# Kernel tuning notes

Hardware: AMD Instinct MI355X
Metric: run time of the kernel (lower is better)

The kernel has to match this reference:

```python
import jax, jax.numpy as jnp
import numpy as np

D_MODEL = 1024
N_HEADS = 16
D_K = D_MODEL // N_HEADS
D_FF = 4096
EPS = 1e-5


def _layernorm(x, g, b):
    mu = jnp.mean(x, axis=-1, keepdims=True)
    var = jnp.mean(jnp.square(x - mu), axis=-1, keepdims=True)
    return (x - mu) * jax.lax.rsqrt(var + EPS) * g + b


def setup_inputs() -> dict:
    key = jax.random.key(0)
    ks = jax.random.split(key, 16)
    s = 0.02
    B, S = 2, 2048
    inp = {
        "x": jax.random.normal(ks[0], (B, S, D_MODEL), dtype=jnp.float32),
        "mask": jnp.ones((1, 1, S, S), dtype=jnp.int32),
        # attention projections (stored [in, out]; y = x @ W + b)
        "Wq": jax.random.normal(ks[1], (D_MODEL, D_MODEL)) * s,
        "bq": jnp.zeros((D_MODEL,)),
        "Wk": jax.random.normal(ks[2], (D_MODEL, D_MODEL)) * s,
        "bk": jnp.zeros((D_MODEL,)),
        "Wv": jax.random.normal(ks[3], (D_MODEL, D_MODEL)) * s,
        "bv": jnp.zeros((D_MODEL,)),
        "Wo": jax.random.normal(ks[4], (D_MODEL, D_MODEL)) * s,
        "bo": jnp.zeros((D_MODEL,)),
        "temperature": jnp.sqrt(jnp.array([float(D_K)], dtype=jnp.float32)),
        "time_weights": jax.random.normal(ks[5], (1, N_HEADS, 1, D_K)),
        "gateW": jax.random.normal(ks[6], (D_K, 1)) * s,
        "gateb": jnp.zeros((1,)),
        "ln_attn_g": jnp.ones((D_MODEL,)),
        "ln_attn_b": jnp.zeros((D_MODEL,)),
        # feed-forward
        "fc1W": jax.random.normal(ks[7], (D_MODEL, D_FF)) * s,
        "fc1b": jnp.zeros((D_FF,)),
        "fc2W": jax.random.normal(ks[8], (D_FF, D_MODEL)) * s,
        "fc2b": jnp.zeros((D_MODEL,)),
        "n1g": jnp.ones((D_MODEL,)),
        "n1b": jnp.zeros((D_MODEL,)),
        "n2g": jnp.ones((D_MODEL,)),
        "n2b": jnp.zeros((D_MODEL,)),
    }
    return inp


def reference(x, mask, Wq, bq, Wk, bk, Wv, bv, Wo, bo, temperature,
              time_weights, gateW, gateb, ln_attn_g, ln_attn_b,
              fc1W, fc1b, fc2W, fc2b, n1g, n1b, n2g, n2b):
    B, S, D = x.shape
    H, dk = N_HEADS, D_K

    def heads(t):  # [B,S,D] -> [B,H,S,dk]
        return t.reshape(B, S, H, dk).transpose(0, 2, 1, 3)

    q = heads(x @ Wq + bq) + time_weights  # learned per-head bias on Q
    k = heads(x @ Wk + bk)
    v = heads(x @ Wv + bv)

    scores = jnp.einsum("bhqd,bhkd->bhqk", q, k) / temperature
    scores = jnp.where(mask == 0, jnp.float32(-1e9), scores)
    gate = jax.nn.sigmoid(q @ gateW + gateb)  # [B,H,S,1] per-query gate
    scores = scores * gate
    probs = jax.nn.softmax(scores, axis=-1)

    ctx = jnp.einsum("bhqk,bhkd->bhqd", probs, v)
    ctx = ctx.transpose(0, 2, 1, 3).reshape(B, S, D)
    attn_out = _layernorm(ctx @ Wo + bo, ln_attn_g, ln_attn_b)

    x1 = _layernorm(x + attn_out, n1g, n1b)
    ff = jax.nn.gelu(x1 @ fc1W + fc1b, approximate=False) @ fc2W + fc2b
    return _layernorm(x1 + ff, n2g, n2b)
```

## Files before the change

kernel.cpp:

```cpp
#include <hip/hip_runtime.h>
#include <stdint.h>
#include <math.h>


typedef uint16_t u16;
typedef unsigned long long u64;
typedef __attribute__((ext_vector_type(8))) short short8;
typedef __attribute__((ext_vector_type(4))) float f32x4;

#define S_LEN 2048
#define DM 1024

#define GLOAD_LDS16(g, l)                                                      \
  __builtin_amdgcn_global_load_lds(                                            \
      (const __attribute__((address_space(1))) void*)(g),                      \
      (__attribute__((address_space(3))) void*)(l), 16, 0, 0)

#define VM0_BARRIER()                                                          \
  do {                                                                         \
    asm volatile("s_waitcnt vmcnt(0)" ::: "memory");                           \
    __builtin_amdgcn_s_barrier();                                              \
  } while (0)

__device__ __forceinline__ float bf2f(u16 h) {
  union { uint32_t u; float f; } x;
  x.u = ((uint32_t)h) << 16;
  return x.f;
}
__device__ __forceinline__ u16 f2bf(float f) {
  union { float f; uint32_t u; } x;
  x.f = f;
  uint32_t r = (x.u + 0x7fffu + ((x.u >> 16) & 1u)) >> 16;
  return (u16)r;
}
__device__ __forceinline__ u16 f2bf_fast(float f) {
  union { float f; uint32_t u; } x;
  x.f = f;
  return (u16)((x.u + 0x8000u) >> 16);
}

__device__ __forceinline__ float gelu_ex(float v) {
  float x = fabsf(v) * 0.70710678118654752f;
  float t = __builtin_amdgcn_rcpf(__builtin_fmaf(0.3275911f, x, 1.0f));
  float p = 1.061405429f;
  p = __builtin_fmaf(p, t, -1.453152027f);
  p = __builtin_fmaf(p, t, 1.421413741f);
  p = __builtin_fmaf(p, t, -0.284496736f);
  p = __builtin_fmaf(p, t, 0.254829592f);
  p = p * t;
  float ex = __builtin_amdgcn_exp2f(-1.4426950408889634f * x * x);
  float er = __builtin_fmaf(-p, ex, 1.0f);
  er = (v < 0.f) ? -er : er;
  return 0.5f * v * (1.0f + er);
}

union U8 { uint4 u; u16 s[8]; };
union U4 { uint2 u; u16 s[4]; };

__global__ __launch_bounds__(256) void cvt_k(const float* __restrict__ in,
                                             u16* __restrict__ out, int n) {
  int i = (blockIdx.x * 256 + threadIdx.x) * 4;
  if (i >= n) return;
  float4 v = *(const float4*)(in + i);
  U4 o;
  o.s[0] = f2bf(v.x); o.s[1] = f2bf(v.y); o.s[2] = f2bf(v.z); o.s[3] = f2bf(v.w);
  *(uint2*)(out + i) = o.u;
}

__global__ __launch_bounds__(256) void mb_k(const int* __restrict__ mask,
                                            u16* __restrict__ mb) {
  int tid = blockIdx.x * 256 + threadIdx.x;
  const int* src = mask + (size_t)tid * 16;
  uint32_t b = 0;
#pragma unroll
  for (int q = 0; q < 4; q++) {
    int4 m = *(const int4*)(src + q * 4);
    b |= (m.x != 0 ? 1u : 0u) << (q * 4 + 0);
    b |= (m.y != 0 ? 1u : 0u) << (q * 4 + 1);
    b |= (m.z != 0 ? 1u : 0u) << (q * 4 + 2);
    b |= (m.w != 0 ? 1u : 0u) << (q * 4 + 3);
  }
  mb[tid] = (u16)b;
}

__device__ __forceinline__ void tcvt_body(const float* __restrict__ in,
                                          u16* __restrict__ out, int R, int C) {
  __shared__ u16 tile[64][72];
  int c0 = blockIdx.x * 64, r0 = blockIdx.y * 64;
  int t = threadIdx.x;
  int r = t & 63, seg = t >> 6;
  const float* src = in + (size_t)(r0 + r) * C + c0 + seg * 16;
#pragma unroll
  for (int q = 0; q < 4; q++) {
    float4 v = *(const float4*)(src + q * 4);
    tile[r][seg * 16 + q * 4 + 0] = f2bf(v.x);
    tile[r][seg * 16 + q * 4 + 1] = f2bf(v.y);
    tile[r][seg * 16 + q * 4 + 2] = f2bf(v.z);
    tile[r][seg * 16 + q * 4 + 3] = f2bf(v.w);
  }
  __syncthreads();
  U8 v0, v1;
#pragma unroll
  for (int i = 0; i < 8; i++) v0.s[i] = tile[seg * 16 + i][r];
#pragma unroll
  for (int i = 0; i < 8; i++) v1.s[i] = tile[seg * 16 + 8 + i][r];
  u16* dst = out + (size_t)(c0 + r) * R + r0 + seg * 16;
  *(uint4*)dst = v0.u;
  *(uint4*)(dst + 8) = v1.u;
}

__global__ __launch_bounds__(256) void transpose_cvt_k(const float* __restrict__ in,
                                                       u16* __restrict__ out,
                                                       int R, int C) {
  tcvt_body(in, out, R, C);
}

__global__ __launch_bounds__(256) void transpose_cvt3_k(const float* __restrict__ i0,
                                                        const float* __restrict__ i1,
                                                        const float* __restrict__ i2,
                                                        u16* __restrict__ o0,
                                                        u16* __restrict__ o1,
                                                        u16* __restrict__ o2) {
  int z = blockIdx.z;
  const float* in = (z == 0) ? i0 : (z == 1) ? i1 : i2;
  u16* out = (z == 0) ? o0 : (z == 1) ? o1 : o2;
  tcvt_body(in, out, 1024, 1024);
}

__global__ __launch_bounds__(256) void vtrans_k(const u16* __restrict__ V,
                                                u16* __restrict__ VT) {
  __shared__ u16 tile[64][72];
  int bx = blockIdx.x, bh = blockIdx.y;
  int b = bh >> 4, h = bh & 15;
  int t = threadIdx.x, r = t & 63, seg = t >> 6;
  const u16* src = V + (size_t)(b * S_LEN + bx * 64 + r) * DM + h * 64 + seg * 16;
  *(uint4*)&tile[r][seg * 16] = *(const uint4*)src;
  *(uint4*)&tile[r][seg * 16 + 8] = *(const uint4*)(src + 8);
  __syncthreads();
  U8 v0, v1;
#pragma unroll
  for (int i = 0; i < 8; i++) v0.s[i] = tile[seg * 16 + i][r];
#pragma unroll
  for (int i = 0; i < 8; i++) v1.s[i] = tile[seg * 16 + 8 + i][r];
  u16* dst = VT + ((size_t)bh * 64 + r) * S_LEN + bx * 64 + seg * 16;
  *(uint4*)dst = v0.u;
  *(uint4*)(dst + 8) = v1.u;
}

template <int BM, int EPI, int MXS>
__global__ __launch_bounds__(256) void gemm_bt(const u16* __restrict__ A,
                                               const u16* __restrict__ Bt,
                                               u16* __restrict__ C,
                                               const float* __restrict__ bias,
                                               int M, int N, int K) {
  constexpr int MI = BM / 32;
  constexpr int RPW = BM / 4;
  __shared__ u16 As[2][BM * 32];
  __shared__ u16 Bs[2][128 * 32];
  int t = threadIdx.x;
  int wid = t >> 6, lane = t & 63;
  int g = lane >> 4, li = lane & 15;
  int bx = MXS ? blockIdx.y : blockIdx.x;
  int by = MXS ? blockIdx.x : blockIdx.y;
  int wr = (wid >> 1) * (BM / 2), wc = (wid & 1) * 64;

  const u16* a0 = A + (size_t)(by * BM + wid * RPW + (lane >> 2)) * K + (lane & 3) * 8;
  const u16* b0 = Bt + (size_t)(bx * 128 + wid * 32 + (lane >> 2)) * K + (lane & 3) * 8;
  u16* lA[2] = {&As[0][wid * RPW * 32], &As[1][wid * RPW * 32]};
  u16* lB[2] = {&Bs[0][wid * 1024], &Bs[1][wid * 1024]};

  f32x4 acc[MI][4];
#pragma unroll
  for (int i = 0; i < MI; i++)
#pragma unroll
    for (int j = 0; j < 4; j++) acc[i][j] = (f32x4){0.f, 0.f, 0.f, 0.f};

  auto stage = [&](int buf, int kk) {
    GLOAD_LDS16(a0 + kk, lA[buf]);
    if (BM == 128) GLOAD_LDS16(a0 + (size_t)16 * K + kk, lA[buf] + 512);
    GLOAD_LDS16(b0 + kk, lB[buf]);
    GLOAD_LDS16(b0 + (size_t)16 * K + kk, lB[buf] + 512);
  };
  auto compute = [&](int buf) {
    short8 af[MI], bfv[4];
#pragma unroll
    for (int i = 0; i < MI; i++)
      af[i] = *(const short8*)&As[buf][(wr + i * 16 + li) * 32 + g * 8];
#pragma unroll
    for (int i = 0; i < 4; i++)
      bfv[i] = *(const short8*)&Bs[buf][(wc + i * 16 + li) * 32 + g * 8];
    __builtin_amdgcn_s_setprio(1);
#pragma unroll
    for (int mi = 0; mi < MI; mi++)
#pragma unroll
      for (int ni = 0; ni < 4; ni++)
        acc[mi][ni] = __builtin_amdgcn_mfma_f32_16x16x32_bf16(
            af[mi], bfv[ni], acc[mi][ni], 0, 0, 0);
    __builtin_amdgcn_s_setprio(0);
  };

  stage(0, 0);
  VM0_BARRIER();
  for (int k0 = 0; k0 < K; k0 += 64) {
    stage(1, k0 + 32);
    compute(0);
    VM0_BARRIER();
    if (k0 + 64 < K) stage(0, k0 + 64);
    compute(1);
    VM0_BARRIER();
  }

#pragma unroll
  for (int ni = 0; ni < 4; ni++) {
    int col = bx * 128 + wc + ni * 16 + li;
    float bv = bias[col];
#pragma unroll
    for (int mi = 0; mi < MI; mi++) {
#pragma unroll
      for (int r = 0; r < 4; r++) {
        int row = by * BM + wr + mi * 16 + g * 4 + r;
        float v = acc[mi][ni][r] + bv;
        if (EPI == 2) v = gelu_ex(v);
        C[(size_t)row * N + col] = f2bf(v);
      }
    }
  }
}

__global__ __launch_bounds__(256) void qkv_gemm(const u16* __restrict__ A,
                                                const u16* __restrict__ WTq,
                                                const u16* __restrict__ WTk,
                                                const u16* __restrict__ WTv,
                                                u16* __restrict__ Cq,
                                                u16* __restrict__ Ck,
                                                u16* __restrict__ Cv,
                                                const float* __restrict__ bq,
                                                const float* __restrict__ bk,
                                                const float* __restrict__ bv,
                                                const float* __restrict__ tw) {
  const int K = 1024, N = 1024;
  __shared__ u16 As[2][128 * 32];
  __shared__ u16 Bs[2][128 * 32];
  int t = threadIdx.x;
  int wid = t >> 6, lane = t & 63;
  int g = lane >> 4, li = lane & 15;
  int by = blockIdx.x, bx = blockIdx.y, z = blockIdx.z;
  int wr = (wid >> 1) * 64, wc = (wid & 1) * 64;

  const u16* Bt = (z == 0) ? WTq : (z == 1) ? WTk : WTv;
  u16* C = (z == 0) ? Cq : (z == 1) ? Ck : Cv;
  const float* bias = (z == 0) ? bq : (z == 1) ? bk : bv;

  const u16* a0 = A + (size_t)(by * 128 + wid * 32 + (lane >> 2)) * K + (lane & 3) * 8;
  const u16* b0 = Bt + (size_t)(bx * 128 + wid * 32 + (lane >> 2)) * K + (lane & 3) * 8;
  u16* lA[2] = {&As[0][wid * 1024], &As[1][wid * 1024]};
  u16* lB[2] = {&Bs[0][wid * 1024], &Bs[1][wid * 1024]};

  f32x4 acc[4][4];
#pragma unroll
  for (int i = 0; i < 4; i++)
#pragma unroll
    for (int j = 0; j < 4; j++) acc[i][j] = (f32x4){0.f, 0.f, 0.f, 0.f};

  auto stage = [&](int buf, int kk) {
    GLOAD_LDS16(a0 + kk, lA[buf]);
    GLOAD_LDS16(a0 + (size_t)16 * K + kk, lA[buf] + 512);
    GLOAD_LDS16(b0 + kk, lB[buf]);
    GLOAD_LDS16(b0 + (size_t)16 * K + kk, lB[buf] + 512);
  };
  auto compute = [&](int buf) {
    short8 af[4], bfv[4];
#pragma unroll
    for (int i = 0; i < 4; i++)
      af[i] = *(const short8*)&As[buf][(wr + i * 16 + li) * 32 + g * 8];
#pragma unroll
    for (int i = 0; i < 4; i++)
      bfv[i] = *(const short8*)&Bs[buf][(wc + i * 16 + li) * 32 + g * 8];
    __builtin_amdgcn_s_setprio(1);
#pragma unroll
    for (int mi = 0; mi < 4; mi++)
#pragma unroll
      for (int ni = 0; ni < 4; ni++)
        acc[mi][ni] = __builtin_amdgcn_mfma_f32_16x16x32_bf16(
            af[mi], bfv[ni], acc[mi][ni], 0, 0, 0);
    __builtin_amdgcn_s_setprio(0);
  };

  stage(0, 0);
  VM0_BARRIER();
  for (int k0 = 0; k0 < K; k0 += 64) {
    stage(1, k0 + 32);
    compute(0);
    VM0_BARRIER();
    if (k0 + 64 < K) stage(0, k0 + 64);
    compute(1);
    VM0_BARRIER();
  }

#pragma unroll
  for (int ni = 0; ni < 4; ni++) {
    int col = bx * 128 + wc + ni * 16 + li;
    float bvv = bias[col];
    if (z == 0) bvv += tw[col];
#pragma unroll
    for (int mi = 0; mi < 4; mi++) {
#pragma unroll
      for (int r = 0; r < 4; r++) {
        int row = by * 128 + wr + mi * 16 + g * 4 + r;
        C[(size_t)row * N + col] = f2bf(acc[mi][ni][r] + bvv);
      }
    }
  }
}

__global__ __launch_bounds__(256) void attn_k(const u16* __restrict__ Q,
                                              const u16* __restrict__ Kp,
                                              const u16* __restrict__ VT,
                                              u16* __restrict__ CTX,
                                              const u16* __restrict__ mb,
                                              const float* __restrict__ gateW,
                                              const float* __restrict__ gateb,
                                              const float* __restrict__ temp) {
  __shared__ u16 Qs[64][72];
  __shared__ u16 Ks[64][72];
  __shared__ u16 Vs[64][72];
  __shared__ u16 Ps[4][16][72];
  __shared__ float gate_s[64];

  int blk = blockIdx.x;
  int bh = blk & 31, qt = blk >> 5;
  int b = bh >> 4, h = bh & 15;
  int t = threadIdx.x, wid = t >> 6, lane = t & 63;
  int g = lane >> 4, li = lane & 15;
  int sq0 = qt * 64;

  const u16* Qb  = Q + ((size_t)b * S_LEN) * DM + h * 64;
  const u16* Kb  = Kp + ((size_t)b * S_LEN) * DM + h * 64;
  const u16* VTb = VT + ((size_t)(b * 16 + h) * 64) * S_LEN;

  {
    int r = t >> 2, cs = (t & 3) * 16;
    const u16* src = Qb + (size_t)(sq0 + r) * DM + cs;
    *(uint4*)&Qs[r][cs] = *(const uint4*)src;
    *(uint4*)&Qs[r][cs + 8] = *(const uint4*)(src + 8);
  }
  __syncthreads();
  if (t < 64) {
    float acc = gateb[0];
#pragma unroll
    for (int d = 0; d < 64; d++) acc += bf2f(Qs[t][d]) * gateW[d];
    gate_s[t] = 1.f / (1.f + __expf(-acc));
  }
  __syncthreads();

  const float LOG2E = 1.4426950408889634f;
  float invt2 = LOG2E / temp[0];
  const float NEG2 = -1.0e9f * 1.4426950408889634f;
  short8 qf0 = *(const short8*)&Qs[wid * 16 + li][g * 8];
  short8 qf1 = *(const short8*)&Qs[wid * 16 + li][32 + g * 8];
  float gqs[4], ng[4];
  int sq[4];
#pragma unroll
  for (int r = 0; r < 4; r++) {
    float gq = gate_s[wid * 16 + g * 4 + r];
    gqs[r] = gq * invt2;
    ng[r] = NEG2 * gq;
    sq[r] = sq0 + wid * 16 + g * 4 + r;
  }

  float m_i[4], psl[4];
  f32x4 o[4];
#pragma unroll
  for (int r = 0; r < 4; r++) { m_i[r] = -1e30f; psl[r] = 0.f; }
#pragma unroll
  for (int n = 0; n < 4; n++) o[n] = (f32x4){0.f, 0.f, 0.f, 0.f};

  for (int kt = 0; kt < 32; kt++) {
    __syncthreads();
    {
      int r = t >> 2, cs = (t & 3) * 16;
      const u16* srcK = Kb + (size_t)(kt * 64 + r) * DM + cs;
      *(uint4*)&Ks[r][cs] = *(const uint4*)srcK;
      *(uint4*)&Ks[r][cs + 8] = *(const uint4*)(srcK + 8);
      const u16* srcV = VTb + (size_t)r * S_LEN + kt * 64 + cs;
      *(uint4*)&Vs[r][cs] = *(const uint4*)srcV;
      *(uint4*)&Vs[r][cs + 8] = *(const uint4*)(srcV + 8);
    }
    u64 bits[4];
#pragma unroll
    for (int r = 0; r < 4; r++)
      bits[r] = *(const u64*)(mb + (size_t)sq[r] * 128 + kt * 4);
    __syncthreads();

    f32x4 sc[4];
#pragma unroll
    for (int ni = 0; ni < 4; ni++) {
      sc[ni] = (f32x4){0.f, 0.f, 0.f, 0.f};
      short8 kf0 = *(const short8*)&Ks[ni * 16 + li][g * 8];
      short8 kf1 = *(const short8*)&Ks[ni * 16 + li][32 + g * 8];
      sc[ni] = __builtin_amdgcn_mfma_f32_16x16x32_bf16(qf0, kf0, sc[ni], 0, 0, 0);
      sc[ni] = __builtin_amdgcn_mfma_f32_16x16x32_bf16(qf1, kf1, sc[ni], 0, 0, 0);
    }

    float sval[4][4];
    float rmax[4] = {-1e30f, -1e30f, -1e30f, -1e30f};
    bool allm = ((bits[0] & bits[1] & bits[2] & bits[3]) == ~0ull);
    if (__all(allm)) {
#pragma unroll
      for (int ni = 0; ni < 4; ni++)
#pragma unroll
        for (int r = 0; r < 4; r++) {
          float s = sc[ni][r] * gqs[r];
          sval[ni][r] = s;
          rmax[r] = fmaxf(rmax[r], s);
        }
    } else {
      u64 bs[4];
#pragma unroll
      for (int r = 0; r < 4; r++) bs[r] = bits[r] >> li;
#pragma unroll
      for (int ni = 0; ni < 4; ni++)
#pragma unroll
        for (int r = 0; r < 4; r++) {
          float s = ((bs[r] >> (ni * 16)) & 1ull) ? sc[ni][r] * gqs[r] : ng[r];
          sval[ni][r] = s;
          rmax[r] = fmaxf(rmax[r], s);
        }
    }
#pragma unroll
    for (int off = 1; off < 16; off <<= 1)
#pragma unroll
      for (int r = 0; r < 4; r++)
        rmax[r] = fmaxf(rmax[r], __shfl_xor(rmax[r], off, 64));

    float alpha[4];
#pragma unroll
    for (int r = 0; r < 4; r++) {
      float mnew = fmaxf(m_i[r], rmax[r]);
      alpha[r] = __builtin_amdgcn_exp2f(m_i[r] - mnew);
      m_i[r] = mnew;
    }
    float pp[4] = {0.f, 0.f, 0.f, 0.f};
#pragma unroll
    for (int ni = 0; ni < 4; ni++)
#pragma unroll
      for (int r = 0; r < 4; r++) {
        float p = __builtin_amdgcn_exp2f(sval[ni][r] - m_i[r]);
        pp[r] += p;
        Ps[wid][g * 4 + r][ni * 16 + li] = f2bf_fast(p);
      }
#pragma unroll
    for (int r = 0; r < 4; r++) psl[r] = psl[r] * alpha[r] + pp[r];
#pragma unroll
    for (int n = 0; n < 4; n++)
#pragma unroll
      for (int r = 0; r < 4; r++) o[n][r] *= alpha[r];

    __builtin_amdgcn_wave_barrier();

    short8 pf0 = *(const short8*)&Ps[wid][li][g * 8];
    short8 pf1 = *(const short8*)&Ps[wid][li][32 + g * 8];
#pragma unroll
    for (int ni = 0; ni < 4; ni++) {
      short8 vf0 = *(const short8*)&Vs[ni * 16 + li][g * 8];
      short8 vf1 = *(const short8*)&Vs[ni * 16 + li][32 + g * 8];
      o[ni] = __builtin_amdgcn_mfma_f32_16x16x32_bf16(pf0, vf0, o[ni], 0, 0, 0);
      o[ni] = __builtin_amdgcn_mfma_f32_16x16x32_bf16(pf1, vf1, o[ni], 0, 0, 0);
    }
  }

  float linv[4];
#pragma unroll
  for (int r = 0; r < 4; r++) {
    float l = psl[r];
#pragma unroll
    for (int off = 1; off < 16; off <<= 1) l += __shfl_xor(l, off, 64);
    linv[r] = 1.f / l;
  }
#pragma unroll
  for (int ni = 0; ni < 4; ni++) {
    int col = h * 64 + ni * 16 + li;
#pragma unroll
    for (int r = 0; r < 4; r++) {
      size_t row = (size_t)b * S_LEN + sq[r];
      CTX[row * DM + col] = f2bf(o[ni][r] * linv[r]);
    }
  }
}

__device__ __forceinline__ void block_sum2(float& a, float& b, float* red, int t) {
#pragma unroll
  for (int off = 32; off > 0; off >>= 1) {
    a += __shfl_xor(a, off, 64);
    b += __shfl_xor(b, off, 64);
  }
  __syncthreads();
  if ((t & 63) == 0) {
    red[(t >> 6) * 2] = a;
    red[(t >> 6) * 2 + 1] = b;
  }
  __syncthreads();
  a = red[0] + red[2] + red[4] + red[6];
  b = red[1] + red[3] + red[5] + red[7];
}

__global__ __launch_bounds__(256) void ln1_k(const u16* __restrict__ po,
                                             const float* __restrict__ x,
                                             const float* __restrict__ g1,
                                             const float* __restrict__ b1,
                                             const float* __restrict__ g2,
                                             const float* __restrict__ b2,
                                             u16* __restrict__ x1) {
  __shared__ float red[8];
  int row = blockIdx.x, t = threadIdx.x;
  size_t base = (size_t)row * 1024 + t * 4;
  U4 pv; pv.u = *(const uint2*)(po + base);
  float v[4];
#pragma unroll
  for (int i = 0; i < 4; i++) v[i] = bf2f(pv.s[i]);
  float s1 = v[0] + v[1] + v[2] + v[3];
  float s2 = v[0]*v[0] + v[1]*v[1] + v[2]*v[2] + v[3]*v[3];
  block_sum2(s1, s2, red, t);
  float mu = s1 * (1.f / 1024.f);
  float rs = rsqrtf(s2 * (1.f / 1024.f) - mu * mu + 1e-5f);
  float4 xv = *(const float4*)(x + base);
  float4 g1v = *(const float4*)(g1 + t * 4);
  float4 b1v = *(const float4*)(b1 + t * 4);
  float w[4];
  w[0] = xv.x + ((v[0] - mu) * rs * g1v.x + b1v.x);
  w[1] = xv.y + ((v[1] - mu) * rs * g1v.y + b1v.y);
  w[2] = xv.z + ((v[2] - mu) * rs * g1v.z + b1v.z);
  w[3] = xv.w + ((v[3] - mu) * rs * g1v.w + b1v.w);
  s1 = w[0] + w[1] + w[2] + w[3];
  s2 = w[0]*w[0] + w[1]*w[1] + w[2]*w[2] + w[3]*w[3];
  block_sum2(s1, s2, red, t);
  mu = s1 * (1.f / 1024.f);
  rs = rsqrtf(s2 * (1.f / 1024.f) - mu * mu + 1e-5f);
  float4 g2v = *(const float4*)(g2 + t * 4);
  float4 b2v = *(const float4*)(b2 + t * 4);
  U4 ov;
  ov.s[0] = f2bf((w[0] - mu) * rs * g2v.x + b2v.x);
  ov.s[1] = f2bf((w[1] - mu) * rs * g2v.y + b2v.y);
  ov.s[2] = f2bf((w[2] - mu) * rs * g2v.z + b2v.z);
  ov.s[3] = f2bf((w[3] - mu) * rs * g2v.w + b2v.w);
  *(uint2*)(x1 + base) = ov.u;
}

__global__ __launch_bounds__(256) void ln2_k(const u16* __restrict__ y,
                                             const u16* __restrict__ x1,
                                             const float* __restrict__ g,
                                             const float* __restrict__ b,
                                             float* __restrict__ out) {
  __shared__ float red[8];
  int row = blockIdx.x, t = threadIdx.x;
  size_t base = (size_t)row * 1024 + t * 4;
  U4 yv; yv.u = *(const uint2*)(y + base);
  U4 xv; xv.u = *(const uint2*)(x1 + base);
  float w[4];
#pragma unroll
  for (int i = 0; i < 4; i++) w[i] = bf2f(yv.s[i]) + bf2f(xv.s[i]);
  float s1 = w[0] + w[1] + w[2] + w[3];
  float s2 = w[0]*w[0] + w[1]*w[1] + w[2]*w[2] + w[3]*w[3];
  block_sum2(s1, s2, red, t);
  float mu = s1 * (1.f / 1024.f);
  float rs = rsqrtf(s2 * (1.f / 1024.f) - mu * mu + 1e-5f);
  float4 gv = *(const float4*)(g + t * 4);
  float4 bv = *(const float4*)(b + t * 4);
  float4 ov;
  ov.x = (w[0] - mu) * rs * gv.x + bv.x;
  ov.y = (w[1] - mu) * rs * gv.y + bv.y;
  ov.z = (w[2] - mu) * rs * gv.z + bv.z;
  ov.w = (w[3] - mu) * rs * gv.w + bv.w;
  *(float4*)(out + base) = ov;
}

extern "C" void kernel_launch(void* const* d_in, const int* in_sizes, int n_in,
                              void* d_out, int out_size, void* d_ws, size_t ws_size,
                              hipStream_t stream) {
  (void)in_sizes; (void)n_in; (void)out_size;
  const float* x    = (const float*)d_in[0];
  const int*   mask = (const int*)d_in[1];
  const float* Wq = (const float*)d_in[2];  const float* bq = (const float*)d_in[3];
  const float* Wk = (const float*)d_in[4];  const float* bk = (const float*)d_in[5];
  const float* Wv = (const float*)d_in[6];  const float* bv = (const float*)d_in[7];
  const float* Wo = (const float*)d_in[8];  const float* bo = (const float*)d_in[9];
  const float* temp = (const float*)d_in[10];
  const float* tw   = (const float*)d_in[11];
  const float* gW   = (const float*)d_in[12]; const float* gb  = (const float*)d_in[13];
  const float* lag  = (const float*)d_in[14]; const float* lab = (const float*)d_in[15];
  const float* f1W  = (const float*)d_in[16]; const float* f1b = (const float*)d_in[17];
  const float* f2W  = (const float*)d_in[18]; const float* f2b = (const float*)d_in[19];
  const float* n1g  = (const float*)d_in[20]; const float* n1b = (const float*)d_in[21];
  const float* n2g  = (const float*)d_in[22]; const float* n2b = (const float*)d_in[23];
  float* out = (float*)d_out;

  u16* ws = (u16*)d_ws;
  const size_t MB4 = (size_t)4096 * 1024;
  u16* s0 = ws;
  u16* s1 = ws + 1 * MB4;
  u16* s2 = ws + 2 * MB4;
  u16* s3 = ws + 3 * MB4;
  u16* s4 = ws + 4 * MB4;
  u16* d0 = (u16*)d_out;
  u16* d1 = d0 + MB4;
  bool bigws = ws_size >= (size_t)9 * 8 * 1024 * 1024;
  u16* Hfull = ws + 5 * MB4;

  dim3 blk(256);
  cvt_k<<<dim3(4096), blk, 0, stream>>>(x, s4, 4096 * 1024);
  transpose_cvt3_k<<<dim3(16, 16, 3), blk, 0, stream>>>(Wq, Wk, Wv, s0, s1, s2);
  qkv_gemm<<<dim3(32, 8, 3), blk, 0, stream>>>(s4, s0, s1, s2, s3, d0, d1,
                                               bq, bk, bv, tw);
  vtrans_k<<<dim3(32, 32), blk, 0, stream>>>(d1, s0);
  mb_k<<<dim3(1024), blk, 0, stream>>>(mask, s1);
  transpose_cvt_k<<<dim3(16, 16), blk, 0, stream>>>(Wo, s4, 1024, 1024);
  attn_k<<<dim3(1024), blk, 0, stream>>>(s3, d0, s0, s2, s1, gW, gb, temp);
  gemm_bt<64, 0, 1><<<dim3(64, 8), blk, 0, stream>>>(s2, s4, d0, bo, 4096, 1024, 1024);
  ln1_k<<<dim3(4096), blk, 0, stream>>>(d0, x, lag, lab, n1g, n1b, s3);
  transpose_cvt_k<<<dim3(64, 16), blk, 0, stream>>>(f1W, s0, 1024, 4096);
  transpose_cvt_k<<<dim3(16, 64), blk, 0, stream>>>(f2W, s1, 4096, 1024);
  if (bigws) {
    gemm_bt<128, 2, 0><<<dim3(32, 32), blk, 0, stream>>>(s3, s0, Hfull, f1b,
                                                         4096, 4096, 1024);
    gemm_bt<64, 0, 0><<<dim3(8, 64), blk, 0, stream>>>(Hfull, s1, s2, f2b,
                                                       4096, 1024, 4096);
  } else {
    for (int i = 0; i < 2; i++) {
      const u16* Ai = s3 + (size_t)i * 2048 * 1024;
      u16* Yi = s2 + (size_t)i * 2048 * 1024;
      gemm_bt<128, 2, 0><<<dim3(32, 16), blk, 0, stream>>>(Ai, s0, d0, f1b,
                                                           2048, 4096, 1024);
      gemm_bt<64, 0, 1><<<dim3(32, 8), blk, 0, stream>>>(d0, s1, Yi, f2b,
                                                         2048, 1024, 4096);
    }
  }
  ln2_k<<<dim3(4096), blk, 0, stream>>>(s2, s3, n2g, n2b, out);
}
```

Measured before the change: 461.3 us.

## Register-prefetch K/V tiles, share Q/P LDS buffer, lazy softmax rescale in attention

The attention kernel now loads the next K/V tile into registers while the current tile is computed, so global-load latency overlaps with MFMA work. The Q tile buffer is reused for the P tile once Q fragments are in registers, which cuts LDS use and allows a launch bound of 5 blocks per CU. The online-softmax rescale is skipped unless some row max rises by more than 8 in log2 units, and the gate dot product is spread over all threads with shuffles. The extra prefetch registers and the threshold-based rescale change register pressure and the numeric path.

```diff
diff --git a/kernel.cpp b/kernel.cpp
--- a/kernel.cpp
+++ b/kernel.cpp
@@ -313,18 +313,17 @@
   }
 }
 
-__global__ __launch_bounds__(256) void attn_k(const u16* __restrict__ Q,
-                                              const u16* __restrict__ Kp,
-                                              const u16* __restrict__ VT,
-                                              u16* __restrict__ CTX,
-                                              const u16* __restrict__ mb,
-                                              const float* __restrict__ gateW,
-                                              const float* __restrict__ gateb,
-                                              const float* __restrict__ temp) {
-  __shared__ u16 Qs[64][72];
+__global__ __launch_bounds__(256, 5) void attn_k(const u16* __restrict__ Q,
+                                                 const u16* __restrict__ Kp,
+                                                 const u16* __restrict__ VT,
+                                                 u16* __restrict__ CTX,
+                                                 const u16* __restrict__ mb,
+                                                 const float* __restrict__ gateW,
+                                                 const float* __restrict__ gateb,
+                                                 const float* __restrict__ temp) {
+  __shared__ u16 QPs[64 * 72];
   __shared__ u16 Ks[64][72];
   __shared__ u16 Vs[64][72];
-  __shared__ u16 Ps[4][16][72];
   __shared__ float gate_s[64];
 
   int blk = blockIdx.x;
@@ -333,40 +332,51 @@
   int t = threadIdx.x, wid = t >> 6, lane = t & 63;
   int g = lane >> 4, li = lane & 15;
   int sq0 = qt * 64;
+  int rr = t >> 2, cc = (t & 3) * 16;
 
   const u16* Qb  = Q + ((size_t)b * S_LEN) * DM + h * 64;
   const u16* Kb  = Kp + ((size_t)b * S_LEN) * DM + h * 64;
   const u16* VTb = VT + ((size_t)(b * 16 + h) * 64) * S_LEN;
 
   {
-    int r = t >> 2, cs = (t & 3) * 16;
-    const u16* src = Qb + (size_t)(sq0 + r) * DM + cs;
-    *(uint4*)&Qs[r][cs] = *(const uint4*)src;
-    *(uint4*)&Qs[r][cs + 8] = *(const uint4*)(src + 8);
+    const u16* src = Qb + (size_t)(sq0 + rr) * DM + cc;
+    *(uint4*)&QPs[rr * 72 + cc] = *(const uint4*)src;
+    *(uint4*)&QPs[rr * 72 + cc + 8] = *(const uint4*)(src + 8);
   }
   __syncthreads();
-  if (t < 64) {
-    float acc = gateb[0];
-#pragma unroll
-    for (int d = 0; d < 64; d++) acc += bf2f(Qs[t][d]) * gateW[d];
-    gate_s[t] = 1.f / (1.f + __expf(-acc));
+  {
+    U8 q0, q1;
+    q0.u = *(const uint4*)&QPs[rr * 72 + cc];
+    q1.u = *(const uint4*)&QPs[rr * 72 + cc + 8];
+    float4 w0 = *(const float4*)(gateW + cc);
+    float4 w1 = *(const float4*)(gateW + cc + 4);
+    float4 w2 = *(const float4*)(gateW + cc + 8);
+    float4 w3 = *(const float4*)(gateW + cc + 12);
+    float acc;
+    acc  = bf2f(q0.s[0]) * w0.x + bf2f(q0.s[1]) * w0.y +
+           bf2f(q0.s[2]) * w0.z + bf2f(q0.s[3]) * w0.w;
+    acc += bf2f(q0.s[4]) * w1.x + bf2f(q0.s[5]) * w1.y +
+           bf2f(q0.s[6]) * w1.z + bf2f(q0.s[7]) * w1.w;
+    acc += bf2f(q1.s[0]) * w2.x + bf2f(q1.s[1]) * w2.y +
+           bf2f(q1.s[2]) * w2.z + bf2f(q1.s[3]) * w2.w;
+    acc += bf2f(q1.s[4]) * w3.x + bf2f(q1.s[5]) * w3.y +
+           bf2f(q1.s[6]) * w3.z + bf2f(q1.s[7]) * w3.w;
+    acc += __shfl_xor(acc, 1, 64);
+    acc += __shfl_xor(acc, 2, 64);
+    if ((t & 3) == 0) gate_s[rr] = 1.f / (1.f + __expf(-(acc + gateb[0])));
   }
   __syncthreads();
 
   const float LOG2E = 1.4426950408889634f;
   float invt2 = LOG2E / temp[0];
-  const float NEG2 = -1.0e9f * 1.4426950408889634f;
-  short8 qf0 = *(const short8*)&Qs[wid * 16 + li][g * 8];
-  short8 qf1 = *(const short8*)&Qs[wid * 16 + li][32 + g * 8];
-  float gqs[4], ng[4];
-  int sq[4];
-#pragma unroll
-  for (int r = 0; r < 4; r++) {
-    float gq = gate_s[wid * 16 + g * 4 + r];
-    gqs[r] = gq * invt2;
-    ng[r] = NEG2 * gq;
-    sq[r] = sq0 + wid * 16 + g * 4 + r;
-  }
+  float cng = -1.0e9f * temp[0];
+  short8 qf0 = *(const short8*)&QPs[(wid * 16 + li) * 72 + g * 8];
+  short8 qf1 = *(const short8*)&QPs[(wid * 16 + li) * 72 + 32 + g * 8];
+  float gqs[4];
+  int row0 = sq0 + wid * 16 + g * 4;
+#pragma unroll
+  for (int r = 0; r < 4; r++) gqs[r] = gate_s[wid * 16 + g * 4 + r] * invt2;
+  const u16* mbp = mb + (size_t)row0 * 128;
 
   float m_i[4], psl[4];
   f32x4 o[4];
@@ -375,21 +385,30 @@
 #pragma unroll
   for (int n = 0; n < 4; n++) o[n] = (f32x4){0.f, 0.f, 0.f, 0.f};
 
+  uint4 kxa, kxb, vxa, vxb;
+  {
+    const u16* sK = Kb + (size_t)rr * DM + cc;
+    kxa = *(const uint4*)sK; kxb = *(const uint4*)(sK + 8);
+    const u16* sV = VTb + (size_t)rr * S_LEN + cc;
+    vxa = *(const uint4*)sV; vxb = *(const uint4*)(sV + 8);
+  }
+
   for (int kt = 0; kt < 32; kt++) {
     __syncthreads();
-    {
-      int r = t >> 2, cs = (t & 3) * 16;
-      const u16* srcK = Kb + (size_t)(kt * 64 + r) * DM + cs;
-      *(uint4*)&Ks[r][cs] = *(const uint4*)srcK;
-      *(uint4*)&Ks[r][cs + 8] = *(const uint4*)(srcK + 8);
-      const u16* srcV = VTb + (size_t)r * S_LEN + kt * 64 + cs;
-      *(uint4*)&Vs[r][cs] = *(const uint4*)srcV;
-      *(uint4*)&Vs[r][cs + 8] = *(const uint4*)(srcV + 8);
-    }
+    *(uint4*)&Ks[rr][cc]     = kxa;
+    *(uint4*)&Ks[rr][cc + 8] = kxb;
+    *(uint4*)&Vs[rr][cc]     = vxa;
+    *(uint4*)&Vs[rr][cc + 8] = vxb;
     u64 bits[4];
 #pragma unroll
     for (int r = 0; r < 4; r++)
-      bits[r] = *(const u64*)(mb + (size_t)sq[r] * 128 + kt * 4);
+      bits[r] = *(const u64*)(mbp + (size_t)r * 128 + kt * 4);
+    if (kt + 1 < 32) {
+      const u16* sK = Kb + (size_t)((kt + 1) * 64 + rr) * DM + cc;
+      kxa = *(const uint4*)sK; kxb = *(const uint4*)(sK + 8);
+      const u16* sV = VTb + (size_t)rr * S_LEN + (kt + 1) * 64 + cc;
+      vxa = *(const uint4*)sV; vxb = *(const uint4*)(sV + 8);
+    }
     __syncthreads();
 
     f32x4 sc[4];
@@ -402,7 +421,6 @@
       sc[ni] = __builtin_amdgcn_mfma_f32_16x16x32_bf16(qf1, kf1, sc[ni], 0, 0, 0);
     }
 
-    float sval[4][4];
     float rmax[4] = {-1e30f, -1e30f, -1e30f, -1e30f};
     bool allm = ((bits[0] & bits[1] & bits[2] & bits[3]) == ~0ull);
     if (__all(allm)) {
@@ -411,7 +429,7 @@
 #pragma unroll
         for (int r = 0; r < 4; r++) {
           float s = sc[ni][r] * gqs[r];
-          sval[ni][r] = s;
+          sc[ni][r] = s;
           rmax[r] = fmaxf(rmax[r], s);
         }
     } else {
@@ -422,8 +440,9 @@
       for (int ni = 0; ni < 4; ni++)
 #pragma unroll
         for (int r = 0; r < 4; r++) {
-          float s = ((bs[r] >> (ni * 16)) & 1ull) ? sc[ni][r] * gqs[r] : ng[r];
-          sval[ni][r] = s;
+          float s = ((bs[r] >> (ni * 16)) & 1ull) ? sc[ni][r] * gqs[r]
+                                                  : gqs[r] * cng;
+          sc[ni][r] = s;
           rmax[r] = fmaxf(rmax[r], s);
         }
     }
@@ -433,33 +452,37 @@
       for (int r = 0; r < 4; r++)
         rmax[r] = fmaxf(rmax[r], __shfl_xor(rmax[r], off, 64));
 
-    float alpha[4];
-#pragma unroll
-    for (int r = 0; r < 4; r++) {
-      float mnew = fmaxf(m_i[r], rmax[r]);
-      alpha[r] = __builtin_amdgcn_exp2f(m_i[r] - mnew);
-      m_i[r] = mnew;
-    }
+    bool need = false;
+#pragma unroll
+    for (int r = 0; r < 4; r++) need = need || (rmax[r] > m_i[r] + 8.f);
+    if (__any(need)) {
+#pragma unroll
+      for (int r = 0; r < 4; r++) {
+        float mnew = fmaxf(m_i[r], rmax[r]);
+        float alpha = __builtin_amdgcn_exp2f(m_i[r] - mnew);
+        m_i[r] = mnew;
+        psl[r] *= alpha;
+#pragma unroll
+        for (int n = 0; n < 4; n++) o[n][r] *= alpha;
+      }
+    }
+
     float pp[4] = {0.f, 0.f, 0.f, 0.f};
 #pragma unroll
     for (int ni = 0; ni < 4; ni++)
 #pragma unroll
       for (int r = 0; r < 4; r++) {
-        float p = __builtin_amdgcn_exp2f(sval[ni][r] - m_i[r]);
+        float p = __builtin_amdgcn_exp2f(sc[ni][r] - m_i[r]);
         pp[r] += p;
-        Ps[wid][g * 4 + r][ni * 16 + li] = f2bf_fast(p);
+        QPs[(wid * 16 + g * 4 + r) * 72 + ni * 16 + li] = f2bf_fast(p);
       }
 #pragma unroll
-    for (int r = 0; r < 4; r++) psl[r] = psl[r] * alpha[r] + pp[r];
-#pragma unroll
-    for (int n = 0; n < 4; n++)
-#pragma unroll
-      for (int r = 0; r < 4; r++) o[n][r] *= alpha[r];
+    for (int r = 0; r < 4; r++) psl[r] += pp[r];
 
     __builtin_amdgcn_wave_barrier();
 
-    short8 pf0 = *(const short8*)&Ps[wid][li][g * 8];
-    short8 pf1 = *(const short8*)&Ps[wid][li][32 + g * 8];
+    short8 pf0 = *(const short8*)&QPs[(wid * 16 + li) * 72 + g * 8];
+    short8 pf1 = *(const short8*)&QPs[(wid * 16 + li) * 72 + 32 + g * 8];
 #pragma unroll
     for (int ni = 0; ni < 4; ni++) {
       short8 vf0 = *(const short8*)&Vs[ni * 16 + li][g * 8];
@@ -482,7 +505,7 @@
     int col = h * 64 + ni * 16 + li;
 #pragma unroll
     for (int r = 0; r < 4; r++) {
-      size_t row = (size_t)b * S_LEN + sq[r];
+      size_t row = (size_t)b * S_LEN + row0 + r;
       CTX[row * DM + col] = f2bf(o[ni][r] * linv[r]);
     }
   }
```

Result: slower. 579.0 us (+25.5%).
